# Performance work log

Hardware: AMD Instinct MI355X
Metric: run time of the kernel (lower is better)

## Reference

```python
import jax, jax.numpy as jnp
import numpy as np

DIM = 1024
NUM_HEADS = 16
HEAD_DIM = DIM // NUM_HEADS
WINDOW = 16
B, S = 2, 8192
MAX_POS = 8192


def setup_inputs() -> dict:
    key = jax.random.key(0)
    ks = jax.random.split(key, 6)
    x = jax.random.normal(ks[0], (B, S, DIM), dtype=jnp.float32)
    # rope angle table [max_pos, head_dim//2]
    rope_freqs = jax.random.uniform(ks[1], (MAX_POS, HEAD_DIM // 2), dtype=jnp.float32)
    scale = 1.0 / np.sqrt(DIM)
    wq = jax.random.normal(ks[2], (DIM, DIM), dtype=jnp.float32) * scale
    wk = jax.random.normal(ks[3], (DIM, DIM), dtype=jnp.float32) * scale
    wv = jax.random.normal(ks[4], (DIM, DIM), dtype=jnp.float32) * scale
    wo = jax.random.normal(ks[5], (DIM, DIM), dtype=jnp.float32) * scale
    return {"x": x, "rope_freqs": rope_freqs, "wq": wq, "wk": wk, "wv": wv, "wo": wo}


def _apply_rope(t, cos, sin):
    # t: [N, W, H, hd]; cos/sin: [1, W, 1, hd//2] (split-half rotation)
    t1, t2 = jnp.split(t, 2, axis=-1)
    return jnp.concatenate([t1 * cos - t2 * sin, t1 * sin + t2 * cos], axis=-1)


def reference(x, rope_freqs, wq, wk, wv, wo):
    Bx, Sx, D = x.shape
    W, H, hd = WINDOW, NUM_HEADS, HEAD_DIM
    n_windows = Sx // W  # S chosen divisible by W (pad = 0 path)
    xw = x.reshape(Bx * n_windows, W, D)
    q = (xw @ wq.T).reshape(Bx * n_windows, W, H, hd)
    k = (xw @ wk.T).reshape(Bx * n_windows, W, H, hd)
    v = (xw @ wv.T).reshape(Bx * n_windows, W, H, hd)
    # position_ids=None path: positions are arange(W) in every window
    freqs = rope_freqs[jnp.arange(W)]                 # [W, hd//2]
    cos = jnp.cos(freqs)[None, :, None, :]
    sin = jnp.sin(freqs)[None, :, None, :]
    q = _apply_rope(q, cos, sin)
    k = _apply_rope(k, cos, sin)
    # non-causal flash attention within each window
    scores = jnp.einsum('nqhd,nkhd->nhqk', q, k) / jnp.sqrt(jnp.float32(hd))
    probs = jax.nn.softmax(scores, axis=-1)
    attn = jnp.einsum('nhqk,nkhd->nqhd', probs, v)    # [B*nw, W, H, hd]
    attn = attn.reshape(Bx, Sx, H * hd)
    return attn @ wo.T
```

## Files before the change

kernel.cpp:

```cpp
#include <hip/hip_runtime.h>
#include <hip/hip_bf16.h>
#include <stdint.h>

typedef short bf16x8 __attribute__((ext_vector_type(8)));
typedef short bf16x4 __attribute__((ext_vector_type(4)));
typedef float f32x4  __attribute__((ext_vector_type(4)));

__device__ __forceinline__ float b2f(short s) {
  union { float f; uint32_t u; } x;
  x.u = ((uint32_t)(uint16_t)s) << 16;
  return x.f;
}
__device__ __forceinline__ short f2b(float f) {
  union { float f; uint32_t u; } x;
  x.f = f;
  uint32_t r = x.u + 0x7fff + ((x.u >> 16) & 1);
  return (short)(r >> 16);
}

__device__ __forceinline__ void gload_lds16(const void* g, void* l) {
  __builtin_amdgcn_global_load_lds(
      (const __attribute__((address_space(1))) void*)g,
      (__attribute__((address_space(3))) void*)l, 16, 0, 0);
}

__global__ __launch_bounds__(256)
void prep(const float* __restrict__ x, const float* __restrict__ rope,
          const float* __restrict__ wq, const float* __restrict__ wk,
          const float* __restrict__ wv, const float* __restrict__ wo,
          short* __restrict__ Xb, short* __restrict__ Wqkv, short* __restrict__ Wob,
          float* __restrict__ costab, float* __restrict__ sintab)
{
  const int64_t XN4 = 16777216 / 4;
  const int64_t WN4 = 1048576 / 4;
  const int64_t total = XN4 + 4 * WN4 + 512;
  for (int64_t i = (int64_t)blockIdx.x * blockDim.x + threadIdx.x; i < total;
       i += (int64_t)gridDim.x * blockDim.x) {
    if (i < XN4) {
      f32x4 v = ((const f32x4*)x)[i];
      bf16x4 o;
#pragma unroll
      for (int j = 0; j < 4; ++j) o[j] = f2b(v[j]);
      ((bf16x4*)Xb)[i] = o;
    } else if (i < XN4 + 3 * WN4) {
      int64_t j = i - XN4;
      const float* src = (j < WN4) ? wq : ((j < 2 * WN4) ? wk : wv);
      int64_t jj = j & (WN4 - 1);
      f32x4 v = ((const f32x4*)src)[jj];
      bf16x4 o;
#pragma unroll
      for (int q = 0; q < 4; ++q) o[q] = f2b(v[q]);
      ((bf16x4*)Wqkv)[j] = o;
    } else if (i < XN4 + 4 * WN4) {
      int64_t j = i - XN4 - 3 * WN4;
      f32x4 v = ((const f32x4*)wo)[j];
      bf16x4 o;
#pragma unroll
      for (int q = 0; q < 4; ++q) o[q] = f2b(v[q]);
      ((bf16x4*)Wob)[j] = o;
    } else {
      int64_t j = i - XN4 - 4 * WN4;
      int pos = (int)(j >> 5), f = (int)(j & 31);
      float a = rope[pos * 32 + f];
      costab[j] = cosf(a);
      sintab[j] = sinf(a);
    }
  }
}

__device__ __forceinline__ void store4(short* C, size_t idx, f32x4 v) {
  bf16x4 o;
#pragma unroll
  for (int j = 0; j < 4; ++j) o[j] = f2b(v[j]);
  *(bf16x4*)(C + idx) = o;
}
__device__ __forceinline__ void store4(float* C, size_t idx, f32x4 v) {
  *(f32x4*)(C + idx) = v;
}

template <typename OutT>
__global__ __launch_bounds__(512, 2)
void gemm_bt3(const short* __restrict__ A, const short* __restrict__ Bw,
              OutT* __restrict__ C, int M, int N, int K, int nmt)
{
  __shared__ __align__(16) char lds[131072];
  const int t = threadIdx.x, lane = t & 63, wid = t >> 6;
  const int wm = wid >> 2, wn = wid & 3;
  const int lr = lane & 15, ls = lane >> 4;

  const int nwg = gridDim.x, bid = blockIdx.x;
  const int swz = (bid & 7) * (nwg >> 3) + (bid >> 3);
  const int mt = swz % nmt, nt = swz / nmt;
  const int m0 = mt << 8, n0 = nt << 8;
  const int T = K >> 6;

  const int srow8 = lane >> 3;
  const int sgr   = (lane & 7) ^ srow8;

  auto stageA = [&](int kt, int rh) {
    char* base = lds + (kt & 1) * 65536;
#pragma unroll
    for (int j = 0; j < 2; ++j) {
      int c  = j * 8 + wid;
      int rb = (c >> 3) * 128 + rh * 64 + (c & 7) * 8;
      gload_lds16(A + (size_t)(m0 + rb + srow8) * K + (kt << 6) + (sgr << 3),
                  base + rb * 128);
    }
  };
  auto stageB = [&](int kt, int ch) {
    char* base = lds + (kt & 1) * 65536 + 32768;
#pragma unroll
    for (int j = 0; j < 2; ++j) {
      int c  = j * 8 + wid;
      int rb = (c >> 2) * 64 + ch * 32 + (c & 3) * 8;
      gload_lds16(Bw + (size_t)(n0 + rb + srow8) * K + (kt << 6) + (sgr << 3),
                  base + rb * 128);
    }
  };

  f32x4 acc[8][4];
#pragma unroll
  for (int m = 0; m < 8; ++m)
#pragma unroll
    for (int n = 0; n < 4; ++n) acc[m][n] = (f32x4){0.f, 0.f, 0.f, 0.f};

  bf16x8 a[2][4], b[2][2];
  auto ldA = [&](int kt, int rh) {
    const char* base = lds + (kt & 1) * 65536;
#pragma unroll
    for (int kk = 0; kk < 2; ++kk)
#pragma unroll
      for (int i = 0; i < 4; ++i) {
        int row = wm * 128 + (rh * 4 + i) * 16 + lr;
        int u = ((kk << 2) + ls) ^ (lr & 7);
        a[kk][i] = *(const bf16x8*)(base + row * 128 + u * 16);
      }
  };
  auto ldB = [&](int kt, int ch) {
    const char* base = lds + (kt & 1) * 65536 + 32768;
#pragma unroll
    for (int kk = 0; kk < 2; ++kk)
#pragma unroll
      for (int j = 0; j < 2; ++j) {
        int row = wn * 64 + (ch * 2 + j) * 16 + lr;
        int u = ((kk << 2) + ls) ^ (lr & 7);
        b[kk][j] = *(const bf16x8*)(base + row * 128 + u * 16);
      }
  };
  auto mfma16 = [&](int rh, int ch) {
    __builtin_amdgcn_s_setprio(1);
#pragma unroll
    for (int kk = 0; kk < 2; ++kk)
#pragma unroll
      for (int i = 0; i < 4; ++i)
#pragma unroll
        for (int j = 0; j < 2; ++j)
          acc[rh * 4 + i][ch * 2 + j] = __builtin_amdgcn_mfma_f32_16x16x32_bf16(
              b[kk][j], a[kk][i], acc[rh * 4 + i][ch * 2 + j], 0, 0, 0);
    __builtin_amdgcn_s_setprio(0);
  };

  stageA(0, 0); stageB(0, 0); stageB(0, 1); stageA(0, 1);
  asm volatile("s_waitcnt vmcnt(4)" ::: "memory");
  __builtin_amdgcn_s_barrier();

  for (int kt = 0; kt < T; ++kt) {
    const bool pf = (kt + 1 < T);
    ldA(kt, 0); ldB(kt, 0);
    if (pf) { stageA(kt + 1, 0); asm volatile("s_waitcnt vmcnt(4)" ::: "memory"); }
    else    {                    asm volatile("s_waitcnt vmcnt(2)" ::: "memory"); }
    asm volatile("s_waitcnt lgkmcnt(8)" ::: "memory");
    __builtin_amdgcn_s_barrier();
    asm volatile("s_waitcnt lgkmcnt(0)" ::: "memory");
    __builtin_amdgcn_sched_barrier(0);
    mfma16(0, 0);
    __builtin_amdgcn_s_barrier();
    ldB(kt, 1);
    if (pf) { stageB(kt + 1, 0); asm volatile("s_waitcnt vmcnt(4)" ::: "memory"); }
    else    {                    asm volatile("s_waitcnt vmcnt(0)" ::: "memory"); }
    __builtin_amdgcn_s_barrier();
    asm volatile("s_waitcnt lgkmcnt(0)" ::: "memory");
    __builtin_amdgcn_sched_barrier(0);
    mfma16(0, 1);
    __builtin_amdgcn_s_barrier();
    ldA(kt, 1);
    if (pf) stageB(kt + 1, 1);
    __builtin_amdgcn_s_barrier();
    asm volatile("s_waitcnt lgkmcnt(0)" ::: "memory");
    __builtin_amdgcn_sched_barrier(0);
    mfma16(1, 1);
    __builtin_amdgcn_s_barrier();
    ldB(kt, 0);
    if (pf) { stageA(kt + 1, 1); asm volatile("s_waitcnt vmcnt(4)" ::: "memory"); }
    __builtin_amdgcn_s_barrier();
    asm volatile("s_waitcnt lgkmcnt(0)" ::: "memory");
    __builtin_amdgcn_sched_barrier(0);
    mfma16(1, 0);
    __builtin_amdgcn_s_barrier();
  }

  const int orow = m0 + wm * 128 + lr;
  const int ocol = n0 + wn * 64 + ls * 4;
#pragma unroll
  for (int m4 = 0; m4 < 8; ++m4)
#pragma unroll
    for (int n4 = 0; n4 < 4; ++n4)
      store4(C, (size_t)(orow + m4 * 16) * N + (ocol + n4 * 16), acc[m4][n4]);
}

__global__ __launch_bounds__(256)
void attn_win(const short* __restrict__ QKV,
              const float* __restrict__ costab, const float* __restrict__ sintab,
              short* __restrict__ Attn)
{
  __shared__ float Plds[4][16][17];
  __shared__ short Vlds[4][16][64];
  const int t = threadIdx.x, lane = t & 63, wid = t >> 6;
  const int pair = blockIdx.x * 4 + wid;
  const int win = pair >> 4, h = pair & 15;
  const int lr = lane & 15;
  const int lk = (lane >> 4) << 3;

  const size_t rowb = (size_t)(win * 16 + lr) * 3072;
  const short* qp = QKV + rowb + h * 64;
  const short* kp = qp + 1024;

  bf16x8 q0 = *(const bf16x8*)(qp + lk);
  bf16x8 q1 = *(const bf16x8*)(qp + 32 + lk);
  bf16x8 k0 = *(const bf16x8*)(kp + lk);
  bf16x8 k1 = *(const bf16x8*)(kp + 32 + lk);

#pragma unroll
  for (int j = 0; j < 2; ++j) {
    int e = (j * 64 + lane) * 8;
    int vr = e >> 6, vc = e & 63;
    *(bf16x8*)&Vlds[wid][vr][vc] =
        *(const bf16x8*)(QKV + (size_t)(win * 16 + vr) * 3072 + 2048 + h * 64 + vc);
  }

  bf16x8 a0, a1, b0, b1;
#pragma unroll
  for (int j = 0; j < 8; ++j) {
    int f = lk + j;
    float c = costab[lr * 32 + f], s = sintab[lr * 32 + f];
    float x1 = b2f(q0[j]), x2 = b2f(q1[j]);
    a0[j] = f2b(x1 * c - x2 * s);
    a1[j] = f2b(x1 * s + x2 * c);
    float y1 = b2f(k0[j]), y2 = b2f(k1[j]);
    b0[j] = f2b(y1 * c - y2 * s);
    b1[j] = f2b(y1 * s + y2 * c);
  }

  f32x4 sc = (f32x4){0.f, 0.f, 0.f, 0.f};
  sc = __builtin_amdgcn_mfma_f32_16x16x32_bf16(a0, b0, sc, 0, 0, 0);
  sc = __builtin_amdgcn_mfma_f32_16x16x32_bf16(a1, b1, sc, 0, 0, 0);

  float p[4];
#pragma unroll
  for (int i = 0; i < 4; ++i) {
    float v = sc[i] * 0.125f;
    float m = v;
#pragma unroll
    for (int msk = 1; msk < 16; msk <<= 1) m = fmaxf(m, __shfl_xor(m, msk));
    float e = __expf(v - m);
    float s = e;
#pragma unroll
    for (int msk = 1; msk < 16; msk <<= 1) s += __shfl_xor(s, msk);
    p[i] = e / s;
  }
#pragma unroll
  for (int i = 0; i < 4; ++i)
    Plds[wid][((lane >> 4) << 2) + i][lr] = p[i];

  __syncthreads();

  const int r = lr, dblk = lane >> 4;
  float a[16];
#pragma unroll
  for (int j = 0; j < 16; ++j) a[j] = 0.f;
#pragma unroll
  for (int k = 0; k < 16; ++k) {
    float pk = Plds[wid][r][k];
    bf16x8 v0 = *(const bf16x8*)&Vlds[wid][k][dblk * 16];
    bf16x8 v1 = *(const bf16x8*)&Vlds[wid][k][dblk * 16 + 8];
#pragma unroll
    for (int j = 0; j < 8; ++j) {
      a[j]     += pk * b2f(v0[j]);
      a[8 + j] += pk * b2f(v1[j]);
    }
  }
  bf16x8 o0, o1;
#pragma unroll
  for (int j = 0; j < 8; ++j) { o0[j] = f2b(a[j]); o1[j] = f2b(a[8 + j]); }
  short* op = Attn + (size_t)(win * 16 + r) * 1024 + h * 64 + dblk * 16;
  *(bf16x8*)op = o0;
  *(bf16x8*)(op + 8) = o1;
}

extern "C" void kernel_launch(void* const* d_in, const int* in_sizes, int n_in,
                              void* d_out, int out_size, void* d_ws, size_t ws_size,
                              hipStream_t stream)
{
  const float* x  = (const float*)d_in[0];
  const float* rf = (const float*)d_in[1];
  const float* wq = (const float*)d_in[2];
  const float* wk = (const float*)d_in[3];
  const float* wv = (const float*)d_in[4];
  const float* wo = (const float*)d_in[5];
  float* out = (float*)d_out;

  char* w = (char*)d_ws;
  short* Xb     = (short*)(w);
  short* Wqkv   = (short*)(w + 33554432);
  short* Wob    = (short*)(w + 39845888);
  short* QKV    = (short*)(w + 41943040);
  short* Attn   = (short*)(w + 142606336);
  float* costab = (float*)(w + 176160768);
  float* sintab = (float*)(w + 176162816);

  prep<<<2048, 256, 0, stream>>>(x, rf, wq, wk, wv, wo, Xb, Wqkv, Wob, costab, sintab);
  gemm_bt3<short><<<768, 512, 0, stream>>>(Xb, Wqkv, QKV, 16384, 3072, 1024, 64);
  attn_win<<<4096, 256, 0, stream>>>(QKV, costab, sintab, Attn);
  gemm_bt3<float><<<256, 512, 0, stream>>>(Attn, Wob, out, 16384, 1024, 1024, 64);
}
```

Measured before the change: 332.2 us.

## Restructure GEMM to 4-stage K=32 pipeline with N-major tile ordering

Replaces the double-buffered K=64 GEMM main loop with a four-slot ring of K=32 tiles, prefetching three steps ahead. Each iteration now runs two MFMA phases instead of four, and the LDS swizzle is changed to fit 64-byte rows. Workgroup tile mapping switches from M-major to N-major, so neighbouring workgroups share A rows. The aim is more memory latency hidden behind compute and fewer barriers per K step, at the cost of more loop iterations, a new swizzle pattern that must stay bank-conflict-free, and different L2 reuse.

```diff
diff --git a/kernel.cpp b/kernel.cpp
--- a/kernel.cpp
+++ b/kernel.cpp
@@ -80,8 +80,8 @@
 
 template <typename OutT>
 __global__ __launch_bounds__(512, 2)
-void gemm_bt3(const short* __restrict__ A, const short* __restrict__ Bw,
-              OutT* __restrict__ C, int M, int N, int K, int nmt)
+void gemm_bt4(const short* __restrict__ A, const short* __restrict__ Bw,
+              OutT* __restrict__ C, int M, int N, int K, int nnt)
 {
   __shared__ __align__(16) char lds[131072];
   const int t = threadIdx.x, lane = t & 63, wid = t >> 6;
@@ -90,31 +90,29 @@
 
   const int nwg = gridDim.x, bid = blockIdx.x;
   const int swz = (bid & 7) * (nwg >> 3) + (bid >> 3);
-  const int mt = swz % nmt, nt = swz / nmt;
+  const int nt = swz % nnt, mt = swz / nnt;
   const int m0 = mt << 8, n0 = nt << 8;
-  const int T = K >> 6;
-
-  const int srow8 = lane >> 3;
-  const int sgr   = (lane & 7) ^ srow8;
-
-  auto stageA = [&](int kt, int rh) {
-    char* base = lds + (kt & 1) * 65536;
+  const int T = K >> 5;
+
+  const int srow = lane >> 2;
+  const int gsrc = (lane & 3) ^ ((lane >> 3) & 3);
+
+  auto stageA = [&](int kt) {
+    char* base = lds + (kt & 3) * 32768;
 #pragma unroll
     for (int j = 0; j < 2; ++j) {
-      int c  = j * 8 + wid;
-      int rb = (c >> 3) * 128 + rh * 64 + (c & 7) * 8;
-      gload_lds16(A + (size_t)(m0 + rb + srow8) * K + (kt << 6) + (sgr << 3),
-                  base + rb * 128);
-    }
-  };
-  auto stageB = [&](int kt, int ch) {
-    char* base = lds + (kt & 1) * 65536 + 32768;
+      int c = j * 8 + wid;
+      gload_lds16(A + (size_t)(m0 + c * 16 + srow) * K + (kt << 5) + (gsrc << 3),
+                  base + c * 1024);
+    }
+  };
+  auto stageB = [&](int kt) {
+    char* base = lds + (kt & 3) * 32768 + 16384;
 #pragma unroll
     for (int j = 0; j < 2; ++j) {
-      int c  = j * 8 + wid;
-      int rb = (c >> 2) * 64 + ch * 32 + (c & 3) * 8;
-      gload_lds16(Bw + (size_t)(n0 + rb + srow8) * K + (kt << 6) + (sgr << 3),
-                  base + rb * 128);
+      int c = j * 8 + wid;
+      gload_lds16(Bw + (size_t)(n0 + c * 16 + srow) * K + (kt << 5) + (gsrc << 3),
+                  base + c * 1024);
     }
   };
 
@@ -124,78 +122,61 @@
 #pragma unroll
     for (int n = 0; n < 4; ++n) acc[m][n] = (f32x4){0.f, 0.f, 0.f, 0.f};
 
-  bf16x8 a[2][4], b[2][2];
-  auto ldA = [&](int kt, int rh) {
-    const char* base = lds + (kt & 1) * 65536;
-#pragma unroll
-    for (int kk = 0; kk < 2; ++kk)
-#pragma unroll
-      for (int i = 0; i < 4; ++i) {
-        int row = wm * 128 + (rh * 4 + i) * 16 + lr;
-        int u = ((kk << 2) + ls) ^ (lr & 7);
-        a[kk][i] = *(const bf16x8*)(base + row * 128 + u * 16);
-      }
-  };
-  auto ldB = [&](int kt, int ch) {
-    const char* base = lds + (kt & 1) * 65536 + 32768;
-#pragma unroll
-    for (int kk = 0; kk < 2; ++kk)
-#pragma unroll
-      for (int j = 0; j < 2; ++j) {
-        int row = wn * 64 + (ch * 2 + j) * 16 + lr;
-        int u = ((kk << 2) + ls) ^ (lr & 7);
-        b[kk][j] = *(const bf16x8*)(base + row * 128 + u * 16);
-      }
-  };
-  auto mfma16 = [&](int rh, int ch) {
+  const int ug = ((ls ^ ((lr >> 1) & 3)) & 3) * 16;
+
+  bf16x8 av[4], bv[4];
+  auto ldA = [&](int kt, int half) {
+    const char* base = lds + (kt & 3) * 32768;
+#pragma unroll
+    for (int i = 0; i < 4; ++i) {
+      int row = wm * 128 + (half * 4 + i) * 16 + lr;
+      av[i] = *(const bf16x8*)(base + row * 64 + ug);
+    }
+  };
+  auto ldB = [&](int kt) {
+    const char* base = lds + (kt & 3) * 32768 + 16384;
+#pragma unroll
+    for (int j = 0; j < 4; ++j) {
+      int row = wn * 64 + j * 16 + lr;
+      bv[j] = *(const bf16x8*)(base + row * 64 + ug);
+    }
+  };
+  auto mfma16 = [&](int half) {
     __builtin_amdgcn_s_setprio(1);
 #pragma unroll
-    for (int kk = 0; kk < 2; ++kk)
-#pragma unroll
-      for (int i = 0; i < 4; ++i)
-#pragma unroll
-        for (int j = 0; j < 2; ++j)
-          acc[rh * 4 + i][ch * 2 + j] = __builtin_amdgcn_mfma_f32_16x16x32_bf16(
-              b[kk][j], a[kk][i], acc[rh * 4 + i][ch * 2 + j], 0, 0, 0);
+    for (int i = 0; i < 4; ++i)
+#pragma unroll
+      for (int j = 0; j < 4; ++j)
+        acc[half * 4 + i][j] = __builtin_amdgcn_mfma_f32_16x16x32_bf16(
+            bv[j], av[i], acc[half * 4 + i][j], 0, 0, 0);
     __builtin_amdgcn_s_setprio(0);
   };
 
-  stageA(0, 0); stageB(0, 0); stageB(0, 1); stageA(0, 1);
-  asm volatile("s_waitcnt vmcnt(4)" ::: "memory");
+  stageA(0); stageB(0); stageA(1); stageB(1); stageA(2); stageB(2);
+  asm volatile("s_waitcnt vmcnt(8)" ::: "memory");
   __builtin_amdgcn_s_barrier();
 
   for (int kt = 0; kt < T; ++kt) {
-    const bool pf = (kt + 1 < T);
-    ldA(kt, 0); ldB(kt, 0);
-    if (pf) { stageA(kt + 1, 0); asm volatile("s_waitcnt vmcnt(4)" ::: "memory"); }
-    else    {                    asm volatile("s_waitcnt vmcnt(2)" ::: "memory"); }
-    asm volatile("s_waitcnt lgkmcnt(8)" ::: "memory");
+    ldA(kt, 0); ldB(kt);
+    if (kt + 3 < T) stageA(kt + 3);
     __builtin_amdgcn_s_barrier();
     asm volatile("s_waitcnt lgkmcnt(0)" ::: "memory");
     __builtin_amdgcn_sched_barrier(0);
-    mfma16(0, 0);
+    mfma16(0);
     __builtin_amdgcn_s_barrier();
-    ldB(kt, 1);
-    if (pf) { stageB(kt + 1, 0); asm volatile("s_waitcnt vmcnt(4)" ::: "memory"); }
-    else    {                    asm volatile("s_waitcnt vmcnt(0)" ::: "memory"); }
+    ldA(kt, 1);
+    if (kt + 3 < T) {
+      stageB(kt + 3);
+      asm volatile("s_waitcnt vmcnt(8)" ::: "memory");
+    } else if (kt + 2 < T) {
+      asm volatile("s_waitcnt vmcnt(4)" ::: "memory");
+    } else {
+      asm volatile("s_waitcnt vmcnt(0)" ::: "memory");
+    }
     __builtin_amdgcn_s_barrier();
     asm volatile("s_waitcnt lgkmcnt(0)" ::: "memory");
     __builtin_amdgcn_sched_barrier(0);
-    mfma16(0, 1);
-    __builtin_amdgcn_s_barrier();
-    ldA(kt, 1);
-    if (pf) stageB(kt + 1, 1);
-    __builtin_amdgcn_s_barrier();
-    asm volatile("s_waitcnt lgkmcnt(0)" ::: "memory");
-    __builtin_amdgcn_sched_barrier(0);
-    mfma16(1, 1);
-    __builtin_amdgcn_s_barrier();
-    ldB(kt, 0);
-    if (pf) { stageA(kt + 1, 1); asm volatile("s_waitcnt vmcnt(4)" ::: "memory"); }
-    __builtin_amdgcn_s_barrier();
-    asm volatile("s_waitcnt lgkmcnt(0)" ::: "memory");
-    __builtin_amdgcn_sched_barrier(0);
-    mfma16(1, 0);
+    mfma16(1);
     __builtin_amdgcn_s_barrier();
   }
 
@@ -319,7 +300,7 @@
   float* sintab = (float*)(w + 176162816);
 
   prep<<<2048, 256, 0, stream>>>(x, rf, wq, wk, wv, wo, Xb, Wqkv, Wob, costab, sintab);
-  gemm_bt3<short><<<768, 512, 0, stream>>>(Xb, Wqkv, QKV, 16384, 3072, 1024, 64);
+  gemm_bt4<short><<<768, 512, 0, stream>>>(Xb, Wqkv, QKV, 16384, 3072, 1024, 12);
   attn_win<<<4096, 256, 0, stream>>>(QKV, costab, sintab, Attn);
-  gemm_bt3<float><<<256, 512, 0, stream>>>(Attn, Wob, out, 16384, 1024, 1024, 64);
-}
+  gemm_bt4<float><<<256, 512, 0, stream>>>(Attn, Wob, out, 16384, 1024, 1024, 4);
+}
```

Result: slower. 339.0 us (+2.0%).
